# Optimization experiments

Hardware: AMD Instinct MI355X
Metric: run time of the kernel (lower is better)

Reference implementation:

```python
import jax, jax.numpy as jnp
import numpy as np

V, D, HID, HEADS = 50000, 128, 128, 4
N, E, G = 100000, 1600000, 256
CH = HID // HEADS  # per-head channels for layer 1


def setup_inputs() -> dict:
    key = jax.random.key(0)
    ks = jax.random.split(key, 16)
    g = lambda i, shape, scale=0.05: jax.random.normal(ks[i], shape, jnp.float32) * scale
    return {
        "x_lex": jax.random.randint(ks[0], (N,), 0, V),
        "edge_index": jax.random.randint(ks[1], (2, E), 0, N),
        "batch": jnp.sort(jax.random.randint(ks[2], (N,), 0, G)),
        "emb": g(3, (V, D)),
        "W1": g(4, (D, HID)), "a1_src": g(5, (HEADS, CH)), "a1_dst": g(6, (HEADS, CH)), "b1": jnp.zeros((HID,), jnp.float32),
        "W2": g(7, (HID, HID)), "a2_src": g(8, (1, HID)), "a2_dst": g(9, (1, HID)), "b2": jnp.zeros((HID,), jnp.float32),
        "Wc1": g(10, (HID, HID // 2)), "bc1": jnp.zeros((HID // 2,), jnp.float32),
        "Wc2": g(11, (HID // 2, 1)), "bc2": jnp.zeros((1,), jnp.float32),
    }


def gat_layer(x, src, dst, W, a_src, a_dst, b, heads, ch):
    """PyG-style GATConv (v1), concat=True, negative_slope=0.2."""
    n = x.shape[0]
    h = (x @ W).reshape(n, heads, ch)                 # [N,H,C]
    al_s = (h * a_src).sum(-1)                        # [N,H]
    al_d = (h * a_dst).sum(-1)                        # [N,H]
    e = jax.nn.leaky_relu(al_s[src] + al_d[dst], 0.2) # [Etot,H]
    # segment softmax over incoming edges per destination node
    m = jax.ops.segment_max(e, dst, num_segments=n)
    ex = jnp.exp(e - m[dst])
    s = jax.ops.segment_sum(ex, dst, num_segments=n)
    alpha = ex / s[dst]
    out = jax.ops.segment_sum(alpha[:, :, None] * h[src], dst, num_segments=n)  # [N,H,C]
    return out.reshape(n, heads * ch) + b


def reference(x_lex, edge_index, batch, emb, W1, a1_src, a1_dst, b1, W2, a2_src, a2_dst, b2, Wc1, bc1, Wc2, bc2):
    n = x_lex.shape[0]
    loops = jnp.arange(n)  # GATConv adds self-loops by default
    src = jnp.concatenate([edge_index[0], loops])
    dst = jnp.concatenate([edge_index[1], loops])
    x = emb[x_lex]                                               # [N,D]
    h = jax.nn.elu(gat_layer(x, src, dst, W1, a1_src, a1_dst, b1, HEADS, CH))
    h = jax.nn.elu(gat_layer(h, src, dst, W2, a2_src, a2_dst, b2, 1, HID))
    sums = jax.ops.segment_sum(h, batch, num_segments=G)
    cnt = jax.ops.segment_sum(jnp.ones((n,), h.dtype), batch, num_segments=G)
    h_pool = sums / jnp.maximum(cnt, 1.0)[:, None]               # global mean pool [G,HID]
    logits = jax.nn.relu(h_pool @ Wc1 + bc1) @ Wc2 + bc2         # [G,1]
    return (logits, h_pool)
```

## Files before the change

kernel.cpp:

```cpp
#include <hip/hip_runtime.h>
#include <hip/hip_bf16.h>
#include <math.h>

#define P_CHUNK 8192
#define NBKT 1024
#define CAP  4096

typedef float f4 __attribute__((ext_vector_type(4)));

__device__ __forceinline__ float lrelu(float x){ return x < 0.f ? 0.2f*x : x; }
__device__ __forceinline__ float elu_(float x){ return x > 0.f ? x : expm1f(x); }

__global__ __launch_bounds__(256) void p3scatter(const int* __restrict__ ei, int E, int Etot,
                                                 int* __restrict__ bcur, int* __restrict__ tmp){
  __shared__ int lh[NBKT];
  __shared__ int lbase[NBKT];
  int tid = threadIdx.x;
  for (int t = tid; t < NBKT; t += 256) lh[t] = 0;
  __syncthreads();
  int base = blockIdx.x * P_CHUNK;
  for (int j = 0; j < P_CHUNK; j += 256){
    int i = base + j + tid;
    if (i < Etot){
      int dst = (i < E) ? ei[E + i] : (i - E);
      atomicAdd(&lh[dst >> 7], 1);
    }
  }
  __syncthreads();
  for (int t = tid; t < NBKT; t += 256){
    int v = lh[t];
    lbase[t] = v ? atomicAdd(&bcur[t], v) : 0;
  }
  __syncthreads();
  for (int t = tid; t < NBKT; t += 256) lh[t] = 0;
  __syncthreads();
  for (int j = 0; j < P_CHUNK; j += 256){
    int i = base + j + tid;
    if (i < Etot){
      int s, d;
      if (i < E){ s = ei[i]; d = ei[E + i]; } else { s = i - E; d = i - E; }
      int b = d >> 7;
      int r = atomicAdd(&lh[b], 1);
      tmp[b*CAP + lbase[b] + r] = s | ((d & 127) << 17);
    }
  }
}

__global__ __launch_bounds__(256) void p2scan(const int* __restrict__ bcur,
                                              int* __restrict__ bbase,
                                              int Etot, int* __restrict__ off, int N){
  __shared__ int wsum[4];
  __shared__ int runsh;
  int tid = threadIdx.x, lane = tid & 63, w = tid >> 6;
  if (tid == 0) runsh = 0;
  __syncthreads();
  for (int c = 0; c < NBKT; c += 256){
    int v = bcur[c + tid];
    int x = v;
    #pragma unroll
    for (int d = 1; d < 64; d <<= 1){ int y = __shfl_up(x, d); if (lane >= d) x += y; }
    if (lane == 63) wsum[w] = x;
    __syncthreads();
    int wpre = 0;
    for (int i = 0; i < w; i++) wpre += wsum[i];
    int run = runsh;
    bbase[c + tid] = run + wpre + x - v;
    __syncthreads();
    if (tid == 0) runsh = run + wsum[0] + wsum[1] + wsum[2] + wsum[3];
    __syncthreads();
  }
  if (tid == 0) off[N] = Etot;
}

__global__ __launch_bounds__(256) void p4local(const int* __restrict__ tmp,
                                               const int* __restrict__ bbase,
                                               const int* __restrict__ bcnt,
                                               int* __restrict__ off, int* __restrict__ srcs, int N){
  __shared__ int cnt[128];
  __shared__ int offL[128];
  int b = blockIdx.x, tid = threadIdx.x;
  int e0 = bbase[b];
  int ne = bcnt[b];
  const int* slab = tmp + (size_t)b*CAP;
  if (tid < 128) cnt[tid] = 0;
  __syncthreads();
  for (int j = tid; j < ne; j += 256)
    atomicAdd(&cnt[(slab[j] >> 17) & 127], 1);
  __syncthreads();
  if (tid < 64){
    int v0 = cnt[2*tid], v1 = cnt[2*tid + 1];
    int p = v0 + v1;
    int x = p;
    #pragma unroll
    for (int d = 1; d < 64; d <<= 1){ int y = __shfl_up(x, d); if (tid >= d) x += y; }
    int excl = x - p;
    offL[2*tid]     = excl;
    offL[2*tid + 1] = excl + v0;
  }
  __syncthreads();
  if (tid < 128){
    int gd = b*128 + tid;
    if (gd < N) off[gd] = e0 + offL[tid];
    cnt[tid] = 0;
  }
  __syncthreads();
  for (int j = tid; j < ne; j += 256){
    int e = slab[j];
    int d = (e >> 17) & 127;
    int r = atomicAdd(&cnt[d], 1);
    srcs[e0 + offL[d] + r] = e & 0x1FFFF;
  }
}

template<int H, bool GATHER>
__global__ __launch_bounds__(256) void gemm_al(
    const float* __restrict__ X, const int* __restrict__ idx,
    const float* __restrict__ W, const float* __restrict__ asrc,
    const float* __restrict__ adst, float* __restrict__ Hout,
    float* __restrict__ als, float* __restrict__ ald, int n)
{
  __shared__ float xs[64][128];
  int tid = threadIdx.x;
  int tr = tid >> 5, tc = tid & 31;
  int r8 = tr*8, c4 = tc*4;
  int row0 = blockIdx.x * 64;

  #pragma unroll
  for (int j=0;j<8;j++){
    int e = tid + j*256;
    int r = e >> 5, cq = e & 31;
    int gr = row0 + r;
    f4 v = (f4)(0.f);
    if (gr < n){
      int srow = GATHER ? idx[gr] : gr;
      v = *reinterpret_cast<const f4*>(&X[(size_t)srow*128 + cq*4]);
    }
    *reinterpret_cast<f4*>(&xs[r][(cq*4 + 4*r) & 127]) = v;
  }
  __syncthreads();

  float acc[8][4];
  #pragma unroll
  for (int r=0;r<8;r++)
    #pragma unroll
    for (int i=0;i<4;i++) acc[r][i] = 0.f;

  #pragma unroll 4
  for (int kq=0;kq<32;kq++){
    int k0 = kq*4;
    f4 xv[8], wv[4];
    #pragma unroll
    for (int i=0;i<8;i++){
      int rr = r8 + i;
      xv[i] = *reinterpret_cast<const f4*>(&xs[rr][(k0 + 4*rr) & 127]);
    }
    #pragma unroll
    for (int kk=0;kk<4;kk++) wv[kk] = *reinterpret_cast<const f4*>(&W[(size_t)(k0+kk)*128 + c4]);
    #pragma unroll
    for (int kk=0;kk<4;kk++)
      #pragma unroll
      for (int i=0;i<8;i++)
        #pragma unroll
        for (int j=0;j<4;j++)
          acc[i][j] = fmaf(xv[i][kk], wv[kk][j], acc[i][j]);
  }

  const f4 asv = *reinterpret_cast<const f4*>(&asrc[c4]);
  const f4 adv = *reinterpret_cast<const f4*>(&adst[c4]);
  const int GT = 32 / H;
  int hh = tc / GT;

  #pragma unroll
  for (int r=0;r<8;r++){
    int gr = row0 + r8 + r;
    if (gr < n){
      f4 o = { acc[r][0], acc[r][1], acc[r][2], acc[r][3] };
      *reinterpret_cast<f4*>(&Hout[(size_t)gr*128 + c4]) = o;
    }
    float ps = acc[r][0]*asv[0] + acc[r][1]*asv[1] + acc[r][2]*asv[2] + acc[r][3]*asv[3];
    float pd = acc[r][0]*adv[0] + acc[r][1]*adv[1] + acc[r][2]*adv[2] + acc[r][3]*adv[3];
    #pragma unroll
    for (int m=1;m<GT;m<<=1){ ps += __shfl_xor(ps,m); pd += __shfl_xor(pd,m); }
    if ((tc & (GT-1)) == 0 && gr < n){
      als[(size_t)gr*H + hh] = ps;
      ald[(size_t)gr*H + hh] = pd;
    }
  }
}

template<int H>
__global__ __launch_bounds__(256) void aggr(
    const float* __restrict__ h, const float* __restrict__ als,
    const float* __restrict__ ald, const int* __restrict__ srcs,
    const int* __restrict__ off, const float* __restrict__ bias,
    float* __restrict__ out, int n)
{
  __shared__ float s_p[4][64*H];
  __shared__ int   s_s[4][64];
  int tid = threadIdx.x;
  int wid = tid >> 6, lane = tid & 63;
  int d = blockIdx.x*4 + wid;
  if (d >= n) return;
  int half = lane >> 5, ch = lane & 31;
  int c4 = ch*4;
  const int hh = (H==1) ? 0 : (ch >> 3);

  int s0 = off[d], s1 = off[d+1];

  float adv[H];
  #pragma unroll
  for (int q=0;q<H;q++) adv[q] = ald[(size_t)d*H + q];

  float m[H], ssum[H];
  #pragma unroll
  for (int q=0;q<H;q++){ m[q] = -INFINITY; ssum[q] = 0.f; }
  float a0=0.f, a1=0.f, a2=0.f, a3=0.f;

  for (int base = s0; base < s1; base += 64){
    int cl = s1 - base; if (cl > 64) cl = 64;

    int sv = 0;
    float e[H];
    if (lane < cl){
      sv = srcs[base + lane];
      #pragma unroll
      for (int q=0;q<H;q++) e[q] = lrelu(als[(size_t)sv*H + q] + adv[q]);
    } else {
      #pragma unroll
      for (int q=0;q<H;q++) e[q] = -INFINITY;
    }

    float cm[H];
    #pragma unroll
    for (int q=0;q<H;q++) cm[q] = e[q];
    #pragma unroll
    for (int sh=1; sh<64; sh<<=1){
      #pragma unroll
      for (int q=0;q<H;q++) cm[q] = fmaxf(cm[q], __shfl_xor(cm[q], sh));
    }

    float p[H], sc[H];
    #pragma unroll
    for (int q=0;q<H;q++){
      float nm = fmaxf(m[q], cm[q]);
      sc[q] = __expf(m[q] - nm);
      ssum[q] *= sc[q];
      m[q] = nm;
      p[q] = __expf(e[q] - nm);
    }
    float schh = sc[0];
    #pragma unroll
    for (int q=1;q<H;q++) schh = (hh==q) ? sc[q] : schh;
    a0 *= schh; a1 *= schh; a2 *= schh; a3 *= schh;

    float cs[H];
    #pragma unroll
    for (int q=0;q<H;q++) cs[q] = p[q];
    #pragma unroll
    for (int sh=1; sh<64; sh<<=1){
      #pragma unroll
      for (int q=0;q<H;q++) cs[q] += __shfl_xor(cs[q], sh);
    }
    #pragma unroll
    for (int q=0;q<H;q++) ssum[q] += cs[q];

    #pragma unroll
    for (int q=0;q<H;q++) s_p[wid][lane*H + q] = p[q];
    s_s[wid][lane] = sv;

    for (int j = half; j < cl; j += 2){
      int s = s_s[wid][j];
      float w = s_p[wid][j*H + hh];
      const float4 hv = *reinterpret_cast<const float4*>(&h[(size_t)s*128 + c4]);
      a0 = fmaf(w, hv.x, a0);
      a1 = fmaf(w, hv.y, a1);
      a2 = fmaf(w, hv.z, a2);
      a3 = fmaf(w, hv.w, a3);
    }
  }

  a0 += __shfl_xor(a0, 32);
  a1 += __shfl_xor(a1, 32);
  a2 += __shfl_xor(a2, 32);
  a3 += __shfl_xor(a3, 32);

  float den = ssum[0];
  #pragma unroll
  for (int q=1;q<H;q++) den = (hh==q) ? ssum[q] : den;
  float inv = 1.f / den;

  if (half == 0){
    const float4 bv = *reinterpret_cast<const float4*>(&bias[c4]);
    float4 o;
    o.x = elu_(a0*inv + bv.x);
    o.y = elu_(a1*inv + bv.y);
    o.z = elu_(a2*inv + bv.z);
    o.w = elu_(a3*inv + bv.w);
    *reinterpret_cast<float4*>(&out[(size_t)d*128 + c4]) = o;
  }
}

__global__ __launch_bounds__(256) void kpool(const float* __restrict__ act,
    const int* __restrict__ batch, int n, float* __restrict__ pool)
{
  __shared__ int sb[2];
  __shared__ float part[128];
  int g = blockIdx.x, tid = threadIdx.x;
  if (tid == 0){
    int lo=0, hi=n;
    while (lo<hi){ int mid=(lo+hi)>>1; if (batch[mid] < g) lo=mid+1; else hi=mid; }
    sb[0]=lo;
    int lo2=lo, hi2=n;
    while (lo2<hi2){ int mid=(lo2+hi2)>>1; if (batch[mid] < g+1) lo2=mid+1; else hi2=mid; }
    sb[1]=lo2;
  }
  __syncthreads();
  int lo=sb[0], hi=sb[1];
  int c = tid & 127, half = tid >> 7;
  float acc = 0.f;
  for (int i=lo+half; i<hi; i+=2) acc += act[(size_t)i*128 + c];
  if (half == 0) part[c] = acc;
  __syncthreads();
  if (half == 1) part[c] += acc;
  __syncthreads();
  if (half == 0){
    float cnt = (float)(hi-lo);
    pool[(size_t)g*128 + c] = part[c] / fmaxf(cnt, 1.f);
  }
}

__global__ __launch_bounds__(64) void kclassify(const float* __restrict__ pool,
    const float* __restrict__ Wc1, const float* __restrict__ bc1,
    const float* __restrict__ Wc2, const float* __restrict__ bc2,
    float* __restrict__ logits)
{
  int g = blockIdx.x, j = threadIdx.x;
  const float* hp = pool + (size_t)g*128;
  float t = bc1[j];
  #pragma unroll 8
  for (int c=0;c<128;c++) t = fmaf(hp[c], Wc1[c*64+j], t);
  t = fmaxf(t, 0.f) * Wc2[j];
  for (int m=1;m<64;m<<=1) t += __shfl_xor(t, m);
  if (j==0) logits[g] = t + bc2[0];
}

extern "C" void kernel_launch(void* const* d_in, const int* in_sizes, int n_in,
                              void* d_out, int out_size, void* d_ws, size_t ws_size,
                              hipStream_t stream)
{
  const int*   x_lex = (const int*)d_in[0];
  const int*   ei    = (const int*)d_in[1];
  const int*   batch = (const int*)d_in[2];
  const float* emb   = (const float*)d_in[3];
  const float* W1    = (const float*)d_in[4];
  const float* a1s   = (const float*)d_in[5];
  const float* a1d   = (const float*)d_in[6];
  const float* b1    = (const float*)d_in[7];
  const float* W2    = (const float*)d_in[8];
  const float* a2s   = (const float*)d_in[9];
  const float* a2d   = (const float*)d_in[10];
  const float* b2    = (const float*)d_in[11];
  const float* Wc1   = (const float*)d_in[12];
  const float* bc1   = (const float*)d_in[13];
  const float* Wc2   = (const float*)d_in[14];
  const float* bc2   = (const float*)d_in[15];

  int N = in_sizes[0];
  int E = in_sizes[1] / 2;
  int Etot = E + N;
  const int G = 256;

  char* p = (char*)d_ws;
  float* hbuf   = (float*)p;          p += (size_t)N*128*4;
  float* act    = (float*)p;          p += (size_t)N*128*4;
  float* als    = (float*)p;          p += (size_t)N*4*4;
  float* ald    = (float*)p;          p += (size_t)N*4*4;
  int*   off    = (int*)p;            p += (size_t)(N+1)*4;
  int*   srcs   = (int*)p;            p += (size_t)Etot*4;
  int*   bbase  = (int*)p;            p += (NBKT+1)*4;
  int*   bcur   = (int*)p;
  int*   tmp    = (int*)hbuf;

  hipMemsetAsync(bcur, 0, NBKT*4, stream);
  int nblk = (Etot + P_CHUNK - 1) / P_CHUNK;
  int nb   = (N + 127) / 128;
  p3scatter<<<nblk,256,0,stream>>>(ei, E, Etot, bcur, tmp);
  p2scan   <<<1,   256,0,stream>>>(bcur, bbase, Etot, off, N);
  p4local  <<<nb,  256,0,stream>>>(tmp, bbase, bcur, off, srcs, N);

  int gb = (N + 63)/64;
  gemm_al<4,true ><<<gb,256,0,stream>>>(emb, x_lex, W1, a1s, a1d, hbuf, als, ald, N);
  aggr<4><<<(N+3)/4,256,0,stream>>>(hbuf, als, ald, srcs, off, b1, act, N);

  gemm_al<1,false><<<gb,256,0,stream>>>(act, nullptr, W2, a2s, a2d, hbuf, als, ald, N);
  aggr<1><<<(N+3)/4,256,0,stream>>>(hbuf, als, ald, srcs, off, b2, act, N);

  float* out = (float*)d_out;
  kpool<<<G,256,0,stream>>>(act, batch, N, out + G);
  kclassify<<<G,64,0,stream>>>(out + G, Wc1, bc1, Wc2, bc2, out);
}
```

Baseline: 522.7 us.

## Fuse layer-1 GEMM with edge bucket scatter and drop separate scan kernel

Runs the layer-1 embedding GEMM and the CSR bucket-scatter pass in a single horizontally fused launch, with block ranges split between the two jobs so they run concurrently. The scatter buffer moves from hbuf to act so the two jobs do not collide. The single-block prefix-scan kernel is removed; each p4local block now sums the preceding bucket counts itself. The GEMM shared tile also switches from an XOR-style rotation to 132-float padding. This saves launches and serialization, at the cost of redundant per-block prefix sums and a larger shared footprint in the fused kernel.

```diff
diff --git a/kernel.cpp b/kernel.cpp
--- a/kernel.cpp
+++ b/kernel.cpp
@@ -11,14 +11,88 @@
 __device__ __forceinline__ float lrelu(float x){ return x < 0.f ? 0.2f*x : x; }
 __device__ __forceinline__ float elu_(float x){ return x > 0.f ? x : expm1f(x); }
 
-__global__ __launch_bounds__(256) void p3scatter(const int* __restrict__ ei, int E, int Etot,
-                                                 int* __restrict__ bcur, int* __restrict__ tmp){
-  __shared__ int lh[NBKT];
-  __shared__ int lbase[NBKT];
+
+template<int H, bool GATHER>
+__device__ __forceinline__ void gemm_body(float (*xs)[132], int bid,
+    const float* __restrict__ X, const int* __restrict__ idx,
+    const float* __restrict__ W, const float* __restrict__ asrc,
+    const float* __restrict__ adst, float* __restrict__ Hout,
+    float* __restrict__ als, float* __restrict__ ald, int n)
+{
+  int tid = threadIdx.x;
+  int tr = tid >> 5, tc = tid & 31;
+  int r8 = tr*8, c4 = tc*4;
+  int row0 = bid * 64;
+
+  #pragma unroll
+  for (int j=0;j<8;j++){
+    int e = tid + j*256;
+    int r = e >> 5, cq = e & 31;
+    int gr = row0 + r;
+    f4 v = (f4)(0.f);
+    if (gr < n){
+      int srow = GATHER ? idx[gr] : gr;
+      v = *reinterpret_cast<const f4*>(&X[(size_t)srow*128 + cq*4]);
+    }
+    *reinterpret_cast<f4*>(&xs[r][cq*4]) = v;
+  }
+  __syncthreads();
+
+  float acc[8][4];
+  #pragma unroll
+  for (int r=0;r<8;r++)
+    #pragma unroll
+    for (int i=0;i<4;i++) acc[r][i] = 0.f;
+
+  #pragma unroll 4
+  for (int kq=0;kq<32;kq++){
+    int k0 = kq*4;
+    f4 xv[8], wv[4];
+    #pragma unroll
+    for (int i=0;i<8;i++) xv[i] = *reinterpret_cast<const f4*>(&xs[r8+i][k0]);
+    #pragma unroll
+    for (int kk=0;kk<4;kk++) wv[kk] = *reinterpret_cast<const f4*>(&W[(size_t)(k0+kk)*128 + c4]);
+    #pragma unroll
+    for (int kk=0;kk<4;kk++)
+      #pragma unroll
+      for (int i=0;i<8;i++)
+        #pragma unroll
+        for (int j=0;j<4;j++)
+          acc[i][j] = fmaf(xv[i][kk], wv[kk][j], acc[i][j]);
+  }
+
+  const f4 asv = *reinterpret_cast<const f4*>(&asrc[c4]);
+  const f4 adv = *reinterpret_cast<const f4*>(&adst[c4]);
+  const int GT = 32 / H;
+  int hh = tc / GT;
+
+  #pragma unroll
+  for (int r=0;r<8;r++){
+    int gr = row0 + r8 + r;
+    if (gr < n){
+      f4 o = { acc[r][0], acc[r][1], acc[r][2], acc[r][3] };
+      *reinterpret_cast<f4*>(&Hout[(size_t)gr*128 + c4]) = o;
+    }
+    float ps = acc[r][0]*asv[0] + acc[r][1]*asv[1] + acc[r][2]*asv[2] + acc[r][3]*asv[3];
+    float pd = acc[r][0]*adv[0] + acc[r][1]*adv[1] + acc[r][2]*adv[2] + acc[r][3]*adv[3];
+    #pragma unroll
+    for (int m=1;m<GT;m<<=1){ ps += __shfl_xor(ps,m); pd += __shfl_xor(pd,m); }
+    if ((tc & (GT-1)) == 0 && gr < n){
+      als[(size_t)gr*H + hh] = ps;
+      ald[(size_t)gr*H + hh] = pd;
+    }
+  }
+}
+
+__device__ __forceinline__ void p3_body(int* lh, int bid,
+    const int* __restrict__ ei, int E, int Etot,
+    int* __restrict__ bcur, int* __restrict__ tmp)
+{
+  int* lbase = lh + NBKT;
   int tid = threadIdx.x;
   for (int t = tid; t < NBKT; t += 256) lh[t] = 0;
   __syncthreads();
-  int base = blockIdx.x * P_CHUNK;
+  int base = bid * P_CHUNK;
   for (int j = 0; j < P_CHUNK; j += 256){
     int i = base + j + tid;
     if (i < Etot){
@@ -46,69 +120,20 @@
   }
 }
 
-__global__ __launch_bounds__(256) void p2scan(const int* __restrict__ bcur,
-                                              int* __restrict__ bbase,
-                                              int Etot, int* __restrict__ off, int N){
-  __shared__ int wsum[4];
-  __shared__ int runsh;
-  int tid = threadIdx.x, lane = tid & 63, w = tid >> 6;
-  if (tid == 0) runsh = 0;
-  __syncthreads();
-  for (int c = 0; c < NBKT; c += 256){
-    int v = bcur[c + tid];
-    int x = v;
-    #pragma unroll
-    for (int d = 1; d < 64; d <<= 1){ int y = __shfl_up(x, d); if (lane >= d) x += y; }
-    if (lane == 63) wsum[w] = x;
-    __syncthreads();
-    int wpre = 0;
-    for (int i = 0; i < w; i++) wpre += wsum[i];
-    int run = runsh;
-    bbase[c + tid] = run + wpre + x - v;
-    __syncthreads();
-    if (tid == 0) runsh = run + wsum[0] + wsum[1] + wsum[2] + wsum[3];
-    __syncthreads();
-  }
-  if (tid == 0) off[N] = Etot;
-}
-
-__global__ __launch_bounds__(256) void p4local(const int* __restrict__ tmp,
-                                               const int* __restrict__ bbase,
-                                               const int* __restrict__ bcnt,
-                                               int* __restrict__ off, int* __restrict__ srcs, int N){
-  __shared__ int cnt[128];
-  __shared__ int offL[128];
-  int b = blockIdx.x, tid = threadIdx.x;
-  int e0 = bbase[b];
-  int ne = bcnt[b];
-  const int* slab = tmp + (size_t)b*CAP;
-  if (tid < 128) cnt[tid] = 0;
-  __syncthreads();
-  for (int j = tid; j < ne; j += 256)
-    atomicAdd(&cnt[(slab[j] >> 17) & 127], 1);
-  __syncthreads();
-  if (tid < 64){
-    int v0 = cnt[2*tid], v1 = cnt[2*tid + 1];
-    int p = v0 + v1;
-    int x = p;
-    #pragma unroll
-    for (int d = 1; d < 64; d <<= 1){ int y = __shfl_up(x, d); if (tid >= d) x += y; }
-    int excl = x - p;
-    offL[2*tid]     = excl;
-    offL[2*tid + 1] = excl + v0;
-  }
-  __syncthreads();
-  if (tid < 128){
-    int gd = b*128 + tid;
-    if (gd < N) off[gd] = e0 + offL[tid];
-    cnt[tid] = 0;
-  }
-  __syncthreads();
-  for (int j = tid; j < ne; j += 256){
-    int e = slab[j];
-    int d = (e >> 17) & 127;
-    int r = atomicAdd(&cnt[d], 1);
-    srcs[e0 + offL[d] + r] = e & 0x1FFFF;
+__global__ __launch_bounds__(256) void k_gemm1_p3(
+    const float* __restrict__ X, const int* __restrict__ idx,
+    const float* __restrict__ W, const float* __restrict__ asrc,
+    const float* __restrict__ adst, float* __restrict__ Hout,
+    float* __restrict__ als, float* __restrict__ ald, int n, int gb,
+    const int* __restrict__ ei, int E, int Etot,
+    int* __restrict__ bcur, int* __restrict__ tmp)
+{
+  __shared__ __align__(16) char smem[64*132*4];
+  if ((int)blockIdx.x < gb){
+    gemm_body<4,true>(reinterpret_cast<float(*)[132]>(smem), blockIdx.x,
+                      X, idx, W, asrc, adst, Hout, als, ald, n);
+  } else {
+    p3_body(reinterpret_cast<int*>(smem), blockIdx.x - gb, ei, E, Etot, bcur, tmp);
   }
 }
 
@@ -119,72 +144,61 @@
     const float* __restrict__ adst, float* __restrict__ Hout,
     float* __restrict__ als, float* __restrict__ ald, int n)
 {
-  __shared__ float xs[64][128];
-  int tid = threadIdx.x;
-  int tr = tid >> 5, tc = tid & 31;
-  int r8 = tr*8, c4 = tc*4;
-  int row0 = blockIdx.x * 64;
-
-  #pragma unroll
-  for (int j=0;j<8;j++){
-    int e = tid + j*256;
-    int r = e >> 5, cq = e & 31;
-    int gr = row0 + r;
-    f4 v = (f4)(0.f);
-    if (gr < n){
-      int srow = GATHER ? idx[gr] : gr;
-      v = *reinterpret_cast<const f4*>(&X[(size_t)srow*128 + cq*4]);
-    }
-    *reinterpret_cast<f4*>(&xs[r][(cq*4 + 4*r) & 127]) = v;
-  }
-  __syncthreads();
-
-  float acc[8][4];
-  #pragma unroll
-  for (int r=0;r<8;r++)
-    #pragma unroll
-    for (int i=0;i<4;i++) acc[r][i] = 0.f;
-
-  #pragma unroll 4
-  for (int kq=0;kq<32;kq++){
-    int k0 = kq*4;
-    f4 xv[8], wv[4];
-    #pragma unroll
-    for (int i=0;i<8;i++){
-      int rr = r8 + i;
-      xv[i] = *reinterpret_cast<const f4*>(&xs[rr][(k0 + 4*rr) & 127]);
-    }
-    #pragma unroll
-    for (int kk=0;kk<4;kk++) wv[kk] = *reinterpret_cast<const f4*>(&W[(size_t)(k0+kk)*128 + c4]);
-    #pragma unroll
-    for (int kk=0;kk<4;kk++)
-      #pragma unroll
-      for (int i=0;i<8;i++)
-        #pragma unroll
-        for (int j=0;j<4;j++)
-          acc[i][j] = fmaf(xv[i][kk], wv[kk][j], acc[i][j]);
-  }
-
-  const f4 asv = *reinterpret_cast<const f4*>(&asrc[c4]);
-  const f4 adv = *reinterpret_cast<const f4*>(&adst[c4]);
-  const int GT = 32 / H;
-  int hh = tc / GT;
-
-  #pragma unroll
-  for (int r=0;r<8;r++){
-    int gr = row0 + r8 + r;
-    if (gr < n){
-      f4 o = { acc[r][0], acc[r][1], acc[r][2], acc[r][3] };
-      *reinterpret_cast<f4*>(&Hout[(size_t)gr*128 + c4]) = o;
-    }
-    float ps = acc[r][0]*asv[0] + acc[r][1]*asv[1] + acc[r][2]*asv[2] + acc[r][3]*asv[3];
-    float pd = acc[r][0]*adv[0] + acc[r][1]*adv[1] + acc[r][2]*adv[2] + acc[r][3]*adv[3];
-    #pragma unroll
-    for (int m=1;m<GT;m<<=1){ ps += __shfl_xor(ps,m); pd += __shfl_xor(pd,m); }
-    if ((tc & (GT-1)) == 0 && gr < n){
-      als[(size_t)gr*H + hh] = ps;
-      ald[(size_t)gr*H + hh] = pd;
-    }
+  __shared__ float xs[64][132];
+  gemm_body<H,GATHER>(xs, blockIdx.x, X, idx, W, asrc, adst, Hout, als, ald, n);
+}
+
+__global__ __launch_bounds__(256) void p4local(const int* __restrict__ tmp,
+                                               const int* __restrict__ bcnt,
+                                               int* __restrict__ off, int* __restrict__ srcs,
+                                               int N, int Etot){
+  __shared__ int cnt[128];
+  __shared__ int offL[128];
+  __shared__ int wred[4];
+  __shared__ int e0sh;
+  int b = blockIdx.x, tid = threadIdx.x, lane = tid & 63, w = tid >> 6;
+
+  int partial = 0;
+  for (int t = tid; t < b; t += 256) partial += bcnt[t];
+  #pragma unroll
+  for (int sh=1; sh<64; sh<<=1) partial += __shfl_xor(partial, sh);
+  if (lane == 0) wred[w] = partial;
+  if (tid < 128) cnt[tid] = 0;
+  __syncthreads();
+  if (tid == 0){
+    e0sh = wred[0] + wred[1] + wred[2] + wred[3];
+    if (b == 0) off[N] = Etot;
+  }
+  __syncthreads();
+  int e0 = e0sh;
+  int ne = bcnt[b];
+  const int* slab = tmp + (size_t)b*CAP;
+
+  for (int j = tid; j < ne; j += 256)
+    atomicAdd(&cnt[(slab[j] >> 17) & 127], 1);
+  __syncthreads();
+  if (tid < 64){
+    int v0 = cnt[2*tid], v1 = cnt[2*tid + 1];
+    int p = v0 + v1;
+    int x = p;
+    #pragma unroll
+    for (int d = 1; d < 64; d <<= 1){ int y = __shfl_up(x, d); if (tid >= d) x += y; }
+    int excl = x - p;
+    offL[2*tid]     = excl;
+    offL[2*tid + 1] = excl + v0;
+  }
+  __syncthreads();
+  if (tid < 128){
+    int gd = b*128 + tid;
+    if (gd < N) off[gd] = e0 + offL[tid];
+    cnt[tid] = 0;
+  }
+  __syncthreads();
+  for (int j = tid; j < ne; j += 256){
+    int e = slab[j];
+    int d = (e >> 17) & 127;
+    int r = atomicAdd(&cnt[d], 1);
+    srcs[e0 + offL[d] + r] = e & 0x1FFFF;
   }
 }
 
@@ -377,19 +391,17 @@
   float* ald    = (float*)p;          p += (size_t)N*4*4;
   int*   off    = (int*)p;            p += (size_t)(N+1)*4;
   int*   srcs   = (int*)p;            p += (size_t)Etot*4;
-  int*   bbase  = (int*)p;            p += (NBKT+1)*4;
   int*   bcur   = (int*)p;
-  int*   tmp    = (int*)hbuf;
+  int*   tmp    = (int*)act;
 
   hipMemsetAsync(bcur, 0, NBKT*4, stream);
   int nblk = (Etot + P_CHUNK - 1) / P_CHUNK;
   int nb   = (N + 127) / 128;
-  p3scatter<<<nblk,256,0,stream>>>(ei, E, Etot, bcur, tmp);
-  p2scan   <<<1,   256,0,stream>>>(bcur, bbase, Etot, off, N);
-  p4local  <<<nb,  256,0,stream>>>(tmp, bbase, bcur, off, srcs, N);
-
-  int gb = (N + 63)/64;
-  gemm_al<4,true ><<<gb,256,0,stream>>>(emb, x_lex, W1, a1s, a1d, hbuf, als, ald, N);
+  int gb   = (N + 63) / 64;
+  k_gemm1_p3<<<gb + nblk, 256, 0, stream>>>(emb, x_lex, W1, a1s, a1d, hbuf, als, ald, N, gb,
+                                            ei, E, Etot, bcur, tmp);
+  p4local<<<nb, 256, 0, stream>>>(tmp, bcur, off, srcs, N, Etot);
+
   aggr<4><<<(N+3)/4,256,0,stream>>>(hbuf, als, ald, srcs, off, b1, act, N);
 
   gemm_al<1,false><<<gb,256,0,stream>>>(act, nullptr, W2, a2s, a2d, hbuf, als, ald, N);
```

Result: faster. 484.6 us (-7.3%).
